# Performance work log

Measured on AMD Instinct MI355X. Metric: run time of the kernel, lower is better.

## Reference

```python
import jax, jax.numpy as jnp
import numpy as np

OUT_FEATURES = 512
IN_FEATURES = 512


def _unfold_tt(G1, G2):
    # G1: (1, do0, r, di0), G2: (r, do1, 1, di1)
    # einsum 'abcd,cefg->abefdg' then reshape -> (out_features, in_features)
    W = jnp.einsum('abcd,cefg->abefdg', G1, G2)
    return W.reshape(OUT_FEATURES, IN_FEATURES)


def setup_inputs() -> dict:
    key = jax.random.key(0)
    ks = jax.random.split(key, 5)
    std = np.sqrt(2.0 / IN_FEATURES).astype(np.float32)
    x = jax.random.normal(ks[0], (8, 4096, 2 * IN_FEATURES), dtype=jnp.float32)
    G1_R = jax.random.uniform(ks[1], (1, 32, 4, 32), jnp.float32, -std, std)
    G2_R = jax.random.uniform(ks[2], (4, 16, 1, 16), jnp.float32, -std, std)
    G1_I = jax.random.uniform(ks[3], (1, 32, 4, 32), jnp.float32, -std, std)
    G2_I = jax.random.uniform(ks[4], (4, 16, 1, 16), jnp.float32, -std, std)
    bias_real = jnp.zeros((OUT_FEATURES,), jnp.float32)
    bias_imag = jnp.zeros((OUT_FEATURES,), jnp.float32)
    return {"x": x, "G1_R": G1_R, "G2_R": G2_R, "G1_I": G1_I, "G2_I": G2_I,
            "bias_real": bias_real, "bias_imag": bias_imag}


def reference(x, G1_R, G2_R, G1_I, G2_I, bias_real, bias_imag):
    W_real = _unfold_tt(G1_R, G2_R)  # (out, in)
    W_imag = _unfold_tt(G1_I, G2_I)
    x_real, x_imag = jnp.split(x, 2, axis=-1)
    # F.linear(x, W, b) = x @ W.T + b
    out_real = x_real @ W_real.T - x_imag @ W_imag.T + bias_real
    out_imag = x_real @ W_imag.T + x_imag @ W_real.T + bias_imag
    return jnp.concatenate([out_real, out_imag], axis=-1)
```

## Files before the change

kernel.cpp:

```cpp
#include <hip/hip_runtime.h>
#include <hip/hip_bf16.h>
#include <stdint.h>


typedef _Float16 half8 __attribute__((ext_vector_type(8)));
typedef _Float16 half4v __attribute__((ext_vector_type(4)));
typedef float f32x4 __attribute__((ext_vector_type(4)));

typedef __attribute__((address_space(3))) void* lds_ptr_t;
typedef const __attribute__((address_space(1))) void* gbl_ptr_t;

__device__ __forceinline__ void gload_lds16(const void* g, void* s) {
  __builtin_amdgcn_global_load_lds((gbl_ptr_t)g, (lds_ptr_t)s, 16, 0, 0);
}

#define BARF() asm volatile("s_barrier" ::: "memory")
#define PRIO1() __builtin_amdgcn_s_setprio(1)
#define PRIO0() __builtin_amdgcn_s_setprio(0)


__global__ void build_bt(const float* __restrict__ G1R, const float* __restrict__ G2R,
                         const float* __restrict__ G1I, const float* __restrict__ G2I,
                         _Float16* __restrict__ BTimg) {
  int idx = blockIdx.x * 256 + threadIdx.x;
  int kcol = idx & 63;
  int row  = (idx >> 6) & 255;
  int kt   = (idx >> 14) & 15;
  int nt   = idx >> 18;
  int n = nt * 256 + row;
  int k = kt * 64 + kcol;
  int o = n & 511, i = k & 511;
  bool imagOut = n >= 512, kHi = k >= 512;
  const float* G1; const float* G2; float sign = 1.0f;
  if (imagOut == kHi) { G1 = G1R; G2 = G2R; }
  else { G1 = G1I; G2 = G2I; if (!imagOut) sign = -1.0f; }
  int b = o >> 4, e = o & 15, d = i >> 4, g = i & 15;
  float w = 0.0f;
#pragma unroll
  for (int c = 0; c < 4; ++c)
    w += G1[b * 128 + c * 32 + d] * G2[c * 256 + e * 16 + g];
  size_t byteoff = ((size_t)(nt * 16 + kt) << 15) + (size_t)row * 128
                 + ((kcol * 2) ^ ((row & 7) << 4));
  *(_Float16*)((char*)BTimg + byteoff) = (_Float16)(sign * w);
}

__global__ __launch_bounds__(512, 2) void tt_gemm(
    const float* __restrict__ A,
    const _Float16* __restrict__ Bimg,
    const float* __restrict__ bias_r, const float* __restrict__ bias_i,
    float* __restrict__ C) {
  __shared__ __align__(16) _Float16 Als[2][16384];
  __shared__ __align__(16) _Float16 Bls[2][16384];

  const int tid = threadIdx.x;
  const int bid = blockIdx.x;
  const int bid2 = (bid & 7) * 64 + (bid >> 3);
  const int mt = bid2 >> 2, nt = bid2 & 3;

  const int lane = tid & 63, wid = tid >> 6;
  const int wm = wid >> 2, wn = wid & 3;
  const int lr = lane & 15, lq = lane >> 4;

  f32x4 acc[8][4] = {};
  float4 areg[8];
  half8 afr0[4][2], afr1[4][2], bfr0[2][2], bfr1[2][2];

  const float* Abase = A + (size_t)mt * 256 * 1024;
  const char* Bbase = (const char*)Bimg + ((size_t)nt << 19);
  const int arow = tid >> 4;
  const int acg  = tid & 15;
  const int awxor = (arow & 7) << 4;
  const int soff = wid * 1024 + lane * 16;
  const int doff = wid * 1024;

  auto aload = [&](int t) {
#pragma unroll
    for (int ii = 0; ii < 8; ++ii)
      areg[ii] = *(const float4*)(Abase + (size_t)(ii * 32 + arow) * 1024 + t * 64 + acg * 4);
  };
  auto awrite = [&](_Float16* buf) {
#pragma unroll
    for (int ii = 0; ii < 8; ++ii) {
      int row = ii * 32 + arow;
      half4v h = { (_Float16)areg[ii].x, (_Float16)areg[ii].y,
                   (_Float16)areg[ii].z, (_Float16)areg[ii].w };
      *(half4v*)((char*)buf + row * 128 + ((acg * 8) ^ awxor)) = h;
    }
  };
  auto bissue = [&](int t, _Float16* ldsbuf) {
    const char* s = Bbase + ((size_t)t << 15) + soff;
    char* d = (char*)ldsbuf + doff;
#pragma unroll
    for (int j = 0; j < 4; ++j)
      gload_lds16(s + j * 8192, d + j * 8192);
  };
  auto lda = [&](const _Float16* buf, int mh, half8 (&af)[4][2]) {
#pragma unroll
    for (int mf = 0; mf < 4; ++mf)
#pragma unroll
      for (int kk = 0; kk < 2; ++kk) {
        int row = wm * 128 + mh * 64 + mf * 16 + lr;
        int byte = row * 128 + ((kk * 64 + lq * 16) ^ ((row & 7) << 4));
        af[mf][kk] = *(const half8*)((const char*)buf + byte);
      }
  };
  auto ldb = [&](const _Float16* buf, int nh, half8 (&bf)[2][2]) {
#pragma unroll
    for (int j = 0; j < 2; ++j)
#pragma unroll
      for (int kk = 0; kk < 2; ++kk) {
        int row = wn * 64 + (nh * 2 + j) * 16 + lr;
        int byte = row * 128 + ((kk * 64 + lq * 16) ^ ((row & 7) << 4));
        bf[j][kk] = *(const half8*)((const char*)buf + byte);
      }
  };
  auto mmaq = [&](half8 (&af)[4][2], half8 (&bf)[2][2], int mb, int nb) {
#pragma unroll
    for (int mf = 0; mf < 4; ++mf)
#pragma unroll
      for (int j = 0; j < 2; ++j)
#pragma unroll
        for (int kk = 0; kk < 2; ++kk)
          acc[mb + mf][nb + j] = __builtin_amdgcn_mfma_f32_16x16x32_f16(
              af[mf][kk], bf[j][kk], acc[mb + mf][nb + j], 0, 0, 0);
  };

  aload(0);
  bissue(0, Bls[0]);
  awrite(Als[0]);
  aload(1);
  asm volatile("s_waitcnt vmcnt(8)" ::: "memory");
  asm volatile("s_waitcnt lgkmcnt(0)" ::: "memory");
  BARF();

  for (int t = 0; t < 16; ++t) {
    const int c = t & 1;
    _Float16* Ac = Als[c];  _Float16* Bc = Bls[c];
    _Float16* An = Als[c ^ 1]; _Float16* Bn = Bls[c ^ 1];
    lda(Ac, 0, afr0); ldb(Bc, 0, bfr0);
    if (t < 15) bissue(t + 1, Bn);
    BARF(); PRIO1(); mmaq(afr0, bfr0, 0, 0); PRIO0(); BARF();
    ldb(Bc, 1, bfr1);
    if (t < 15) awrite(An);
    BARF(); PRIO1(); mmaq(afr0, bfr1, 0, 2); PRIO0(); BARF();
    lda(Ac, 1, afr1);
    if (t < 14) aload(t + 2);
    BARF(); PRIO1(); mmaq(afr1, bfr1, 4, 2); PRIO0(); BARF();
    PRIO1(); mmaq(afr1, bfr0, 4, 0); PRIO0();
    if (t < 14) {
      asm volatile("s_waitcnt vmcnt(8)" ::: "memory");
      asm volatile("s_waitcnt lgkmcnt(0)" ::: "memory");
      BARF();
    } else if (t == 14) {
      asm volatile("s_waitcnt vmcnt(0)" ::: "memory");
      asm volatile("s_waitcnt lgkmcnt(0)" ::: "memory");
      BARF();
    }
  }

  const int row0 = mt * 256, col0 = nt * 256;
#pragma unroll
  for (int fn = 0; fn < 4; ++fn) {
    int col = col0 + wn * 64 + fn * 16 + lr;
    float bias = (col < 512) ? bias_r[col] : bias_i[col - 512];
#pragma unroll
    for (int fm = 0; fm < 8; ++fm) {
      int r0 = row0 + wm * 128 + (fm >> 2) * 64 + (fm & 3) * 16 + lq * 4;
#pragma unroll
      for (int r = 0; r < 4; ++r)
        C[(size_t)(r0 + r) * 1024 + col] = acc[fm][fn][r] + bias;
    }
  }
}

extern "C" void kernel_launch(void* const* d_in, const int* in_sizes, int n_in,
                              void* d_out, int out_size, void* d_ws, size_t ws_size,
                              hipStream_t stream) {
  const float* x   = (const float*)d_in[0];
  const float* G1R = (const float*)d_in[1];
  const float* G2R = (const float*)d_in[2];
  const float* G1I = (const float*)d_in[3];
  const float* G2I = (const float*)d_in[4];
  const float* br  = (const float*)d_in[5];
  const float* bi  = (const float*)d_in[6];
  float* out = (float*)d_out;
  _Float16* Bimg = (_Float16*)d_ws;

  build_bt<<<4096, 256, 0, stream>>>(G1R, G2R, G1I, G2I, Bimg);
  tt_gemm<<<512, 512, 0, stream>>>(x, Bimg, br, bi, out);
}
```

Before: 116.6 us.

## Pre-convert A to swizzled fp16 image and stage both operands via direct-to-LDS loads

Adds a separate kernel that converts the fp32 activations into a pre-swizzled fp16 tile image in workspace. The GEMM then loads both A and B straight into LDS with global_load_lds, removing per-thread register staging and in-loop conversion. The main loop is unrolled by two and the quarter-tile prefetches are interleaved across the MFMA phases with finer waitcnt control. The cost is an extra kernel launch plus an fp32 read and fp16 write of all of x, which is 128 MB read and 64 MB written, and the fp16 image is then read back several times by the GEMM.

```diff
diff --git a/kernel.cpp b/kernel.cpp
--- a/kernel.cpp
+++ b/kernel.cpp
@@ -15,6 +15,9 @@
 }
 
 #define BARF() asm volatile("s_barrier" ::: "memory")
+#define LGKM0() asm volatile("s_waitcnt lgkmcnt(0)" ::: "memory")
+#define VMC6() asm volatile("s_waitcnt vmcnt(6)" ::: "memory")
+#define VMC0() asm volatile("s_waitcnt vmcnt(0)" ::: "memory")
 #define PRIO1() __builtin_amdgcn_s_setprio(1)
 #define PRIO0() __builtin_amdgcn_s_setprio(0)
 
@@ -44,9 +47,25 @@
   *(_Float16*)((char*)BTimg + byteoff) = (_Float16)(sign * w);
 }
 
+__global__ __launch_bounds__(256) void build_at(const float* __restrict__ A,
+                                                _Float16* __restrict__ Aimg) {
+  const int tid = threadIdx.x;
+  const int kt = blockIdx.x & 15, mt = blockIdx.x >> 4;
+  const float* src = A + (size_t)mt * 256 * 1024 + kt * 64;
+  char* dst = (char*)Aimg + ((size_t)(mt * 16 + kt) << 15);
+  const int cg = tid & 15;
+  const int rb = tid >> 4;
+#pragma unroll
+  for (int r = 0; r < 16; ++r) {
+    int row = rb + r * 16;
+    float4 v = *(const float4*)(src + (size_t)row * 1024 + cg * 4);
+    half4v h = { (_Float16)v.x, (_Float16)v.y, (_Float16)v.z, (_Float16)v.w };
+    *(half4v*)(dst + row * 128 + ((cg * 8) ^ ((row & 7) << 4))) = h;
+  }
+}
+
 __global__ __launch_bounds__(512, 2) void tt_gemm(
-    const float* __restrict__ A,
-    const _Float16* __restrict__ Bimg,
+    const _Float16* __restrict__ Aimg, const _Float16* __restrict__ Bimg,
     const float* __restrict__ bias_r, const float* __restrict__ bias_i,
     float* __restrict__ C) {
   __shared__ __align__(16) _Float16 Als[2][16384];
@@ -62,37 +81,16 @@
   const int lr = lane & 15, lq = lane >> 4;
 
   f32x4 acc[8][4] = {};
-  float4 areg[8];
   half8 afr0[4][2], afr1[4][2], bfr0[2][2], bfr1[2][2];
 
-  const float* Abase = A + (size_t)mt * 256 * 1024;
+  const char* Abase = (const char*)Aimg + ((size_t)mt << 19);
   const char* Bbase = (const char*)Bimg + ((size_t)nt << 19);
-  const int arow = tid >> 4;
-  const int acg  = tid & 15;
-  const int awxor = (arow & 7) << 4;
-  const int soff = wid * 1024 + lane * 16;
-  const int doff = wid * 1024;
-
-  auto aload = [&](int t) {
-#pragma unroll
-    for (int ii = 0; ii < 8; ++ii)
-      areg[ii] = *(const float4*)(Abase + (size_t)(ii * 32 + arow) * 1024 + t * 64 + acg * 4);
-  };
-  auto awrite = [&](_Float16* buf) {
-#pragma unroll
-    for (int ii = 0; ii < 8; ++ii) {
-      int row = ii * 32 + arow;
-      half4v h = { (_Float16)areg[ii].x, (_Float16)areg[ii].y,
-                   (_Float16)areg[ii].z, (_Float16)areg[ii].w };
-      *(half4v*)((char*)buf + row * 128 + ((acg * 8) ^ awxor)) = h;
-    }
-  };
-  auto bissue = [&](int t, _Float16* ldsbuf) {
-    const char* s = Bbase + ((size_t)t << 15) + soff;
-    char* d = (char*)ldsbuf + doff;
-#pragma unroll
-    for (int j = 0; j < 4; ++j)
-      gload_lds16(s + j * 8192, d + j * 8192);
+  const int qoff = wid * 1024 + lane * 16;
+  const int qdst = wid * 1024;
+
+  auto stageQ = [&](const char* base, int t, int q, _Float16* buf) {
+    gload_lds16(base + ((size_t)t << 15) + (q << 13) + qoff,
+                (char*)buf + (q << 13) + qdst);
   };
   auto lda = [&](const _Float16* buf, int mh, half8 (&af)[4][2]) {
 #pragma unroll
@@ -125,37 +123,48 @@
               af[mf][kk], bf[j][kk], acc[mb + mf][nb + j], 0, 0, 0);
   };
 
-  aload(0);
-  bissue(0, Bls[0]);
-  awrite(Als[0]);
-  aload(1);
-  asm volatile("s_waitcnt vmcnt(8)" ::: "memory");
-  asm volatile("s_waitcnt lgkmcnt(0)" ::: "memory");
+  _Float16* A0 = Als[0]; _Float16* A1 = Als[1];
+  _Float16* B0 = Bls[0]; _Float16* B1 = Bls[1];
+
+#pragma unroll
+  for (int q = 0; q < 4; ++q) stageQ(Abase, 0, q, A0);
+#pragma unroll
+  for (int q = 0; q < 4; ++q) stageQ(Bbase, 0, q, B0);
+  stageQ(Abase, 1, 0, A1); stageQ(Abase, 1, 2, A1);
+  stageQ(Bbase, 1, 0, B1); stageQ(Bbase, 1, 1, B1);
+  stageQ(Bbase, 1, 2, B1); stageQ(Bbase, 1, 3, B1);
+  VMC6();
   BARF();
 
-  for (int t = 0; t < 16; ++t) {
-    const int c = t & 1;
-    _Float16* Ac = Als[c];  _Float16* Bc = Bls[c];
-    _Float16* An = Als[c ^ 1]; _Float16* Bn = Bls[c ^ 1];
-    lda(Ac, 0, afr0); ldb(Bc, 0, bfr0);
-    if (t < 15) bissue(t + 1, Bn);
-    BARF(); PRIO1(); mmaq(afr0, bfr0, 0, 0); PRIO0(); BARF();
-    ldb(Bc, 1, bfr1);
-    if (t < 15) awrite(An);
-    BARF(); PRIO1(); mmaq(afr0, bfr1, 0, 2); PRIO0(); BARF();
-    lda(Ac, 1, afr1);
-    if (t < 14) aload(t + 2);
-    BARF(); PRIO1(); mmaq(afr1, bfr1, 4, 2); PRIO0(); BARF();
-    PRIO1(); mmaq(afr1, bfr0, 4, 0); PRIO0();
-    if (t < 14) {
-      asm volatile("s_waitcnt vmcnt(8)" ::: "memory");
-      asm volatile("s_waitcnt lgkmcnt(0)" ::: "memory");
-      BARF();
-    } else if (t == 14) {
-      asm volatile("s_waitcnt vmcnt(0)" ::: "memory");
-      asm volatile("s_waitcnt lgkmcnt(0)" ::: "memory");
-      BARF();
-    }
+  for (int i = 0; i < 8; ++i) {
+    const int t1 = 2 * i + 1, t2 = 2 * i + 2, t3 = 2 * i + 3;
+    const bool pf = (i < 7);
+    lda(A0, 0, afr0); ldb(B0, 0, bfr0);
+    stageQ(Abase, t1, 1, A1); stageQ(Abase, t1, 3, A1);
+    BARF(); LGKM0(); PRIO1(); mmaq(afr0, bfr0, 0, 0); PRIO0(); BARF();
+    ldb(B0, 1, bfr1);
+    if (pf) { stageQ(Abase, t2, 0, A0); stageQ(Abase, t2, 2, A0); }
+    BARF(); LGKM0(); PRIO1(); mmaq(afr0, bfr1, 0, 2); PRIO0(); BARF();
+    lda(A0, 1, afr1);
+    if (pf) { stageQ(Bbase, t2, 0, B0); stageQ(Bbase, t2, 1, B0); }
+    BARF(); LGKM0(); PRIO1(); mmaq(afr1, bfr1, 4, 2); PRIO0(); BARF();
+    if (pf) { stageQ(Bbase, t2, 2, B0); stageQ(Bbase, t2, 3, B0); }
+    BARF(); LGKM0(); PRIO1(); mmaq(afr1, bfr0, 4, 0); PRIO0();
+    if (pf) { VMC6(); } else { VMC0(); }
+    BARF();
+    lda(A1, 0, afr0); ldb(B1, 0, bfr0);
+    if (pf) { stageQ(Abase, t2, 1, A0); stageQ(Abase, t2, 3, A0); }
+    BARF(); LGKM0(); PRIO1(); mmaq(afr0, bfr0, 0, 0); PRIO0(); BARF();
+    ldb(B1, 1, bfr1);
+    if (pf) { stageQ(Abase, t3, 0, A1); stageQ(Abase, t3, 2, A1); }
+    BARF(); LGKM0(); PRIO1(); mmaq(afr0, bfr1, 0, 2); PRIO0(); BARF();
+    lda(A1, 1, afr1);
+    if (pf) { stageQ(Bbase, t3, 0, B1); stageQ(Bbase, t3, 1, B1); }
+    BARF(); LGKM0(); PRIO1(); mmaq(afr1, bfr1, 4, 2); PRIO0(); BARF();
+    if (pf) { stageQ(Bbase, t3, 2, B1); stageQ(Bbase, t3, 3, B1); }
+    BARF(); LGKM0(); PRIO1(); mmaq(afr1, bfr0, 4, 0); PRIO0();
+    if (pf) { VMC6(); }
+    BARF();
   }
 
   const int row0 = mt * 256, col0 = nt * 256;
@@ -184,8 +193,11 @@
   const float* br  = (const float*)d_in[5];
   const float* bi  = (const float*)d_in[6];
   float* out = (float*)d_out;
+
   _Float16* Bimg = (_Float16*)d_ws;
+  _Float16* Aimg = (_Float16*)((char*)d_ws + (2u << 20));
 
   build_bt<<<4096, 256, 0, stream>>>(G1R, G2R, G1I, G2I, Bimg);
-  tt_gemm<<<512, 512, 0, stream>>>(x, Bimg, br, bi, out);
-}
+  build_at<<<2048, 256, 0, stream>>>(x, Aimg);
+  tt_gemm<<<512, 512, 0, stream>>>(Aimg, Bimg, br, bi, out);
+}
```

After: 129.4 us. 1.11x slower.
